# Kernel tuning notes

Hardware: AMD Instinct MI355X
Metric: run time of the kernel (lower is better)

The kernel has to match this reference:

```python
import jax, jax.numpy as jnp
import numpy as np
import math

IN_FEATURES = 4096
OUT_FEATURES = 4096
P = max(IN_FEATURES, OUT_FEATURES)   # total_permutations
D = min(IN_FEATURES, OUT_FEATURES)   # diag_length
SPARSITY = 0.1
K = math.ceil(int((1.0 - SPARSITY) * IN_FEATURES * OUT_FEATURES) / D)  # 3687
ALPHA_LR = 0.01
NUM_ITER = 50


def sparse_soft_topk_mask_dykstra(alpha, k, l, num_iter):
    """Dykstra projection of alpha/l onto {0<=m<=1, sum(m)=k} (soft top-k mask)."""
    s = alpha / l
    n = s.shape[0]
    p0 = jnp.zeros_like(s)
    q0 = jnp.zeros_like(s)

    def body(carry, _):
        x, p, q = carry
        # project x+p onto hyperplane sum = k
        t = x + p
        y = t + (k - jnp.sum(t)) / n
        p = t - y
        # project y+q onto box [0, 1]
        u = y + q
        x_new = jnp.clip(u, 0.0, 1.0)
        q = u - x_new
        return (x_new, p, q), None

    (x, _, _), _ = jax.lax.scan(body, (s, p0, q0), None, length=num_iter)
    return x  # last projection is onto the box -> exact zeros / ones


def compute_weight(V, alpha):
    a = sparse_soft_topk_mask_dykstra(alpha, K, ALPHA_LR, NUM_ITER)  # (P,)
    vals = a[:, None] * V                                             # (P, D)
    i = jnp.arange(P)[:, None]
    j = jnp.arange(D)[None, :]
    if OUT_FEATURES >= IN_FEATURES:
        # pseudo-diagonal i: rows shifted by i, column j scaled by V[i, j]
        rows = (i + j) % OUT_FEATURES
        cols = jnp.broadcast_to(j, (P, D))
    else:
        # row r scaled by V[i, r], columns shifted by i
        rows = jnp.broadcast_to(j, (P, D))
        cols = (i + j) % IN_FEATURES
    W = jnp.zeros((OUT_FEATURES, IN_FEATURES), V.dtype)
    W = W.at[rows.reshape(-1), cols.reshape(-1)].add(vals.reshape(-1))
    return W


def setup_inputs() -> dict:
    key = jax.random.key(0)
    k1, k2 = jax.random.split(key)
    # kaiming_uniform_(a=sqrt(5)) over fan_in = D -> bound = sqrt(1/D)
    bound = 1.0 / np.sqrt(D)
    V = jax.random.uniform(k1, (P, D), jnp.float32, -bound, bound)
    alpha = jnp.ones((P,), jnp.float32) / IN_FEATURES
    x = jax.random.normal(k2, (512, IN_FEATURES), jnp.float32)
    return {"x": x, "V": V, "alpha": alpha}


def reference(x, V, alpha):
    W = compute_weight(V, alpha)  # (out, in)
    return x @ W.T                # F.linear(x, W)
```

## Files before the change

kernel.cpp:

```cpp
#include <hip/hip_runtime.h>
#include <hip/hip_bf16.h>
#include <stdint.h>

#define PDIM 4096
#define KSEL 3687.0f
#define NITER 50

typedef unsigned short ushort_t;
typedef __attribute__((ext_vector_type(8))) __bf16 bf16x8;
typedef __attribute__((ext_vector_type(4))) float f32x4;

typedef __attribute__((address_space(3))) void lds_void;
typedef __attribute__((address_space(1))) const void glob_void;

__device__ __forceinline__ ushort_t f32_to_bf16_rne(float f) {
  union { float f; uint32_t u; } v; v.f = f;
  uint32_t r = 0x7FFFu + ((v.u >> 16) & 1u);
  return (ushort_t)((v.u + r) >> 16);
}

__device__ __forceinline__ float bf16_to_f32(ushort_t h) {
  union { uint32_t u; float f; } v; v.u = ((uint32_t)h) << 16;
  return v.f;
}

__device__ __forceinline__ void async_cp16(const void* g, void* l) {
  __builtin_amdgcn_global_load_lds((glob_void*)g, (lds_void*)l, 16, 0, 0);
}

__device__ __forceinline__ float wave_sum_dpp(float x) {
  float s = x;
  int t;
  t = __builtin_amdgcn_update_dpp(0, __float_as_int(s), 0x111, 0xF, 0xF, true);
  s += __int_as_float(t);
  t = __builtin_amdgcn_update_dpp(0, __float_as_int(s), 0x112, 0xF, 0xF, true);
  s += __int_as_float(t);
  t = __builtin_amdgcn_update_dpp(0, __float_as_int(s), 0x114, 0xF, 0xF, true);
  s += __int_as_float(t);
  t = __builtin_amdgcn_update_dpp(0, __float_as_int(s), 0x118, 0xF, 0xF, true);
  s += __int_as_float(t);
  t = __builtin_amdgcn_update_dpp(0, __float_as_int(s), 0x142, 0xA, 0xF, true);
  s += __int_as_float(t);
  t = __builtin_amdgcn_update_dpp(0, __float_as_int(s), 0x143, 0xC, 0xF, true);
  s += __int_as_float(t);
  return s;
}

__global__ __launch_bounds__(256) void prep_kernel(
    const float* __restrict__ alpha, float* __restrict__ a_out,
    const float* __restrict__ x, ushort_t* __restrict__ Xb, int n4,
    const float* __restrict__ V) {
  if (blockIdx.x >= 1 && blockIdx.x <= 2048) {
    const float4* V4 = (const float4*)V;
    const int base = (blockIdx.x - 1) * 2048 + (int)threadIdx.x;
#pragma unroll
    for (int i = 0; i < 8; ++i) {
      const float4 vv = V4[base + i * 256];
      asm volatile("" :: "v"(vv.x), "v"(vv.y), "v"(vv.z), "v"(vv.w));
    }
    return;
  }
  if (blockIdx.x != 0) {
    const int i = (blockIdx.x - 2049) * 256 + threadIdx.x;
    if (i < n4) {
      const float4 v = ((const float4*)x)[i];
      ushort4 o;
      o.x = f32_to_bf16_rne(v.x);
      o.y = f32_to_bf16_rne(v.y);
      o.z = f32_to_bf16_rne(v.z);
      o.w = f32_to_bf16_rne(v.w);
      ((ushort4*)Xb)[i] = o;
    }
    return;
  }
  __shared__ float red[8];
  const int tid = threadIdx.x;
  const int lane = tid & 63;
  const int wv = tid >> 6;
  float xx[16], q[16];
  float p = 0.0f;
#pragma unroll
  for (int i = 0; i < 16; ++i) {
    xx[i] = alpha[i * 256 + tid] * 100.0f;
    q[i] = 0.0f;
  }
  for (int it = 0; it < NITER; ++it) {
    float t[16];
    float loc = 0.0f;
#pragma unroll
    for (int i = 0; i < 16; ++i) { t[i] = xx[i] + p; loc += t[i]; }
    loc = wave_sum_dpp(loc);
    const int slot = (it & 1) * 4;
    if (lane == 63) red[slot + wv] = loc;
    __syncthreads();
    const float tot = red[slot] + red[slot + 1] + red[slot + 2] + red[slot + 3];
    const float corr = (KSEL - tot) * (1.0f / 4096.0f);
    p = -corr;
#pragma unroll
    for (int i = 0; i < 16; ++i) {
      const float y = t[i] + corr;
      const float u = y + q[i];
      const float xn = fminf(fmaxf(u, 0.0f), 1.0f);
      q[i] = u - xn;
      xx[i] = xn;
    }
  }
#pragma unroll
  for (int i = 0; i < 16; ++i) a_out[i * 256 + tid] = xx[i];
}

__global__ __launch_bounds__(256) void wmat_kernel(
    const float* __restrict__ V, const float* __restrict__ a,
    ushort_t* __restrict__ Wb) {
  __shared__ float vt[192][67];
  const int t = threadIdx.x;
  const int r0 = blockIdx.x * 128;
  const int c0 = blockIdx.y * 64;
  const int dbase = (r0 - c0 - 63 + 2 * PDIM) & (PDIM - 1);
  const int csub = (t & 15) * 4;
  const int rsub = t >> 4;
#pragma unroll
  for (int i = 0; i < 12; ++i) {
    const int ld = i * 16 + rsub;
    const int d = (dbase + ld) & (PDIM - 1);
    const float av = a[d];
    const float4 vv = *(const float4*)(V + (size_t)d * PDIM + c0 + csub);
    vt[ld][csub + 0] = av * vv.x;
    vt[ld][csub + 1] = av * vv.y;
    vt[ld][csub + 2] = av * vv.z;
    vt[ld][csub + 3] = av * vv.w;
  }
  __syncthreads();
#pragma unroll
  for (int k = 0; k < 4; ++k) {
    const int ry = (t >> 3) + k * 32;
    const int cb = (t & 7) * 8;
    ushort_t pk[8];
#pragma unroll
    for (int j = 0; j < 8; ++j) {
      const int c = cb + j;
      pk[j] = f32_to_bf16_rne(vt[ry - c + 63][c]);
    }
    *(uint4*)(Wb + (size_t)(r0 + ry) * PDIM + c0 + cb) = *(const uint4*)pk;
  }
}

__global__ __launch_bounds__(256, 3) void gemm_kernel(
    const ushort_t* __restrict__ Xb, const ushort_t* __restrict__ Wb,
    ushort_t* __restrict__ par) {
  constexpr int Kdim = 4096, KQ = 1024;
  __shared__ __align__(16) ushort_t As[128 * 64];
  __shared__ __align__(16) ushort_t Bs[128 * 64];
  const int tid = threadIdx.x;
  const int lane = tid & 63;
  const int w = tid >> 6;
  const int l15 = lane & 15;
  const int quad = lane >> 4;
  const int z = blockIdx.x;
  const int nblk = blockIdx.y;
  const int mblk = blockIdx.z;
  const int m0 = mblk * 128;
  const int n0 = nblk * 128;
  const int kbase = z * KQ;
  const int arow = lane >> 3;
  const int aslot = lane & 7;

  f32x4 acc[8][2];
#pragma unroll
  for (int mt = 0; mt < 8; ++mt)
#pragma unroll
    for (int nt = 0; nt < 2; ++nt) acc[mt][nt] = (f32x4){0.f, 0.f, 0.f, 0.f};

  for (int it = 0; it < KQ / 64; ++it) {
    const int k0 = kbase + it * 64;
#pragma unroll
    for (int s = w; s < 16; s += 4) {
      const int row = s * 8 + arow;
      const int j = aslot ^ (row & 7);
      async_cp16(Xb + (size_t)(m0 + row) * Kdim + k0 + j * 8,
                 (char*)As + (size_t)s * 1024);
      async_cp16(Wb + (size_t)(n0 + row) * Kdim + k0 + j * 8,
                 (char*)Bs + (size_t)s * 1024);
    }
    __syncthreads();
#pragma unroll
    for (int kk = 0; kk < 64; kk += 32) {
      const int cj = (kk >> 3) + quad;
      bf16x8 bfv[2];
#pragma unroll
      for (int nt = 0; nt < 2; ++nt) {
        const int row = w * 32 + nt * 16 + l15;
        bfv[nt] = *(const bf16x8*)&Bs[(row * 8 + (cj ^ (row & 7))) * 8];
      }
#pragma unroll
      for (int mt = 0; mt < 8; ++mt) {
        const int row = mt * 16 + l15;
        const bf16x8 af = *(const bf16x8*)&As[(row * 8 + (cj ^ (row & 7))) * 8];
        acc[mt][0] = __builtin_amdgcn_mfma_f32_16x16x32_bf16(af, bfv[0],
                                                             acc[mt][0], 0, 0, 0);
        acc[mt][1] = __builtin_amdgcn_mfma_f32_16x16x32_bf16(af, bfv[1],
                                                             acc[mt][1], 0, 0, 0);
      }
    }
    __syncthreads();
  }
  const int tile = nblk * 4 + mblk;
  ushort_t* pbase = par + ((size_t)z * 128 + tile) * 16384;
#pragma unroll
  for (int mt = 0; mt < 8; ++mt) {
#pragma unroll
    for (int nt = 0; nt < 2; ++nt) {
      const int slot = mt * 2 + nt;
      ushort4 o;
      o.x = f32_to_bf16_rne(acc[mt][nt][0]);
      o.y = f32_to_bf16_rne(acc[mt][nt][1]);
      o.z = f32_to_bf16_rne(acc[mt][nt][2]);
      o.w = f32_to_bf16_rne(acc[mt][nt][3]);
      *(ushort4*)(pbase + (size_t)(slot * 256 + tid) * 4) = o;
    }
  }
}

__global__ __launch_bounds__(256) void combine_kernel(
    const ushort_t* __restrict__ par, float* __restrict__ out) {
  const int tile = blockIdx.x >> 2;
  const int qh = blockIdx.x & 3;
  const int nblk = tile >> 2;
  const int mblk = tile & 3;
  const int m0 = mblk * 128;
  const int n0 = nblk * 128;
  const int tid = threadIdx.x;
  const int lane = tid & 63;
  const int w = tid >> 6;
  const int l15 = lane & 15;
  const int quad = lane >> 4;
#pragma unroll
  for (int ss = 0; ss < 4; ++ss) {
    const int slot = qh * 4 + ss;
    float s0 = 0.f, s1 = 0.f, s2 = 0.f, s3 = 0.f;
#pragma unroll
    for (int z = 0; z < 4; ++z) {
      const ushort4 v = *(const ushort4*)(par +
          ((size_t)z * 128 + tile) * 16384 + (size_t)(slot * 256 + tid) * 4);
      s0 += bf16_to_f32(v.x);
      s1 += bf16_to_f32(v.y);
      s2 += bf16_to_f32(v.z);
      s3 += bf16_to_f32(v.w);
    }
    const int mt = slot >> 1;
    const int nt = slot & 1;
    const int mb = m0 + mt * 16 + quad * 4;
    const int n = n0 + w * 32 + nt * 16 + l15;
    out[(size_t)(mb + 0) * PDIM + n] = s0;
    out[(size_t)(mb + 1) * PDIM + n] = s1;
    out[(size_t)(mb + 2) * PDIM + n] = s2;
    out[(size_t)(mb + 3) * PDIM + n] = s3;
  }
}

extern "C" void kernel_launch(void* const* d_in, const int* in_sizes, int n_in,
                              void* d_out, int out_size, void* d_ws,
                              size_t ws_size, hipStream_t stream) {
  const float* x = (const float*)d_in[0];
  const float* V = (const float*)d_in[1];
  const float* alpha = (const float*)d_in[2];
  float* out = (float*)d_out;
  const int M = in_sizes[0] / PDIM;

  float* a_mask = (float*)d_ws;
  ushort_t* Xb = (ushort_t*)((char*)d_ws + 16 * 1024);
  ushort_t* Wb = Xb + (size_t)M * PDIM;
  ushort_t* par = Wb + (size_t)PDIM * PDIM;

  const int n4x = (M * PDIM) / 4;
  prep_kernel<<<1 + 2048 + (n4x + 255) / 256, 256, 0, stream>>>(
      alpha, a_mask, x, Xb, n4x, V);
  wmat_kernel<<<dim3(PDIM / 128, PDIM / 64), 256, 0, stream>>>(V, a_mask, Wb);
  gemm_kernel<<<dim3(4, PDIM / 128, M / 128), 256, 0, stream>>>(Xb, Wb, par);
  combine_kernel<<<512, 256, 0, stream>>>(par, out);
}
```

Baseline: 148.8 us.

## Fuse split-K reduction into GEMM via last-block atomic counter and remap grid

Removes the separate combine kernel. Each GEMM block now bumps a per-tile atomic counter after writing its bf16 partial, and the last of the four split-K blocks sums all partials and writes the fp32 output. The grid becomes 1-D with a swizzled block-to-(z,m,n) mapping, which changes scheduling order and likely L2 reuse. Counters are zeroed in prep_kernel. This saves one launch and its dependency gap, but the reduction now runs serially inside the last block for each tile.

```diff
diff --git a/kernel.cpp b/kernel.cpp
--- a/kernel.cpp
+++ b/kernel.cpp
@@ -49,7 +49,7 @@
 __global__ __launch_bounds__(256) void prep_kernel(
     const float* __restrict__ alpha, float* __restrict__ a_out,
     const float* __restrict__ x, ushort_t* __restrict__ Xb, int n4,
-    const float* __restrict__ V) {
+    const float* __restrict__ V, int* __restrict__ cnt) {
   if (blockIdx.x >= 1 && blockIdx.x <= 2048) {
     const float4* V4 = (const float4*)V;
     const int base = (blockIdx.x - 1) * 2048 + (int)threadIdx.x;
@@ -61,6 +61,7 @@
     return;
   }
   if (blockIdx.x != 0) {
+    if (blockIdx.x == 2049 && threadIdx.x < 128) cnt[threadIdx.x] = 0;
     const int i = (blockIdx.x - 2049) * 256 + threadIdx.x;
     if (i < n4) {
       const float4 v = ((const float4*)x)[i];
@@ -147,18 +148,22 @@
 
 __global__ __launch_bounds__(256, 3) void gemm_kernel(
     const ushort_t* __restrict__ Xb, const ushort_t* __restrict__ Wb,
-    ushort_t* __restrict__ par) {
+    ushort_t* __restrict__ par, float* __restrict__ out,
+    int* __restrict__ cnt) {
   constexpr int Kdim = 4096, KQ = 1024;
   __shared__ __align__(16) ushort_t As[128 * 64];
   __shared__ __align__(16) ushort_t Bs[128 * 64];
+  __shared__ int lastf;
   const int tid = threadIdx.x;
   const int lane = tid & 63;
   const int w = tid >> 6;
   const int l15 = lane & 15;
   const int quad = lane >> 4;
-  const int z = blockIdx.x;
-  const int nblk = blockIdx.y;
-  const int mblk = blockIdx.z;
+  const int bid = blockIdx.x;
+  const int u = ((bid & 7) << 6) | (bid >> 3);
+  const int z = u & 3;
+  const int mblk = (u >> 2) & 3;
+  const int nblk = u >> 4;
   const int m0 = mblk * 128;
   const int n0 = nblk * 128;
   const int kbase = z * KQ;
@@ -219,29 +224,18 @@
       *(ushort4*)(pbase + (size_t)(slot * 256 + tid) * 4) = o;
     }
   }
-}
-
-__global__ __launch_bounds__(256) void combine_kernel(
-    const ushort_t* __restrict__ par, float* __restrict__ out) {
-  const int tile = blockIdx.x >> 2;
-  const int qh = blockIdx.x & 3;
-  const int nblk = tile >> 2;
-  const int mblk = tile & 3;
-  const int m0 = mblk * 128;
-  const int n0 = nblk * 128;
-  const int tid = threadIdx.x;
-  const int lane = tid & 63;
-  const int w = tid >> 6;
-  const int l15 = lane & 15;
-  const int quad = lane >> 4;
-#pragma unroll
-  for (int ss = 0; ss < 4; ++ss) {
-    const int slot = qh * 4 + ss;
+  __threadfence();
+  if (tid == 0) lastf = (atomicAdd(&cnt[tile], 1) == 3);
+  __syncthreads();
+  if (!lastf) return;
+  __threadfence();
+#pragma unroll
+  for (int slot = 0; slot < 16; ++slot) {
     float s0 = 0.f, s1 = 0.f, s2 = 0.f, s3 = 0.f;
 #pragma unroll
-    for (int z = 0; z < 4; ++z) {
+    for (int zz = 0; zz < 4; ++zz) {
       const ushort4 v = *(const ushort4*)(par +
-          ((size_t)z * 128 + tile) * 16384 + (size_t)(slot * 256 + tid) * 4);
+          ((size_t)zz * 128 + tile) * 16384 + (size_t)(slot * 256 + tid) * 4);
       s0 += bf16_to_f32(v.x);
       s1 += bf16_to_f32(v.y);
       s2 += bf16_to_f32(v.z);
@@ -271,11 +265,11 @@
   ushort_t* Xb = (ushort_t*)((char*)d_ws + 16 * 1024);
   ushort_t* Wb = Xb + (size_t)M * PDIM;
   ushort_t* par = Wb + (size_t)PDIM * PDIM;
+  int* cnt = (int*)(par + (size_t)4 * 128 * 16384);
 
   const int n4x = (M * PDIM) / 4;
   prep_kernel<<<1 + 2048 + (n4x + 255) / 256, 256, 0, stream>>>(
-      alpha, a_mask, x, Xb, n4x, V);
+      alpha, a_mask, x, Xb, n4x, V, cnt);
   wmat_kernel<<<dim3(PDIM / 128, PDIM / 64), 256, 0, stream>>>(V, a_mask, Wb);
-  gemm_kernel<<<dim3(4, PDIM / 128, M / 128), 256, 0, stream>>>(Xb, Wb, par);
-  combine_kernel<<<512, 256, 0, stream>>>(par, out);
-}
+  gemm_kernel<<<512, 256, 0, stream>>>(Xb, Wb, par, out, cnt);
+}
```

After: 218.0 us. +46.5%, slower.
